# Optimization experiments

Measured on AMD Instinct MI355X. Metric: run time of the kernel, lower is better.

## Reference

```python
import jax, jax.numpy as jnp
import numpy as np
from jax.scipy.special import gammaln

TEMP = 1.0
PRIOR = 0.2
THRESHOLD = 0.5
EPS = 1e-12


def _normalize(x):
    # F.normalize: x / max(||x||_2, eps)
    n = jnp.linalg.norm(x, axis=-1, keepdims=True)
    return x / jnp.maximum(n, EPS)


def setup_inputs() -> dict:
    key = jax.random.key(0)
    k1, k2 = jax.random.split(key, 2)
    B, L, D = 8, 4096, 512
    hidden = jax.random.normal(k1, (B, L, D), dtype=jnp.float32)
    # uniform noise for RelaxedBernoulli rsample (probs shape is (B, L) after left-pad)
    noise = jax.random.uniform(k2, (B, L), dtype=jnp.float32, minval=1e-6, maxval=1.0 - 1e-6)
    # learned projections, initialized to identity as in the module
    q_w = jnp.eye(D, dtype=jnp.float32)
    k_w = jnp.eye(D, dtype=jnp.float32)
    return {"hidden": hidden, "q_w": q_w, "k_w": k_w, "noise": noise}


def reference(hidden, q_w, k_w, noise):
    B, L, D = hidden.shape
    # cosine-similarity boundary scoring between adjacent tokens
    q = _normalize(hidden[:, :-1]) @ q_w.T  # (B, L-1, D)
    k = _normalize(hidden[:, 1:]) @ k_w.T   # (B, L-1, D)
    cos_sim = jnp.einsum('bld,bld->bl', q, k)  # (B, L-1)
    probs = jnp.clip((1.0 - cos_sim) / 2.0, 0.0, 1.0)
    probs = jnp.pad(probs, ((0, 0), (1, 0)), constant_values=1.0)  # (B, L), first pos always boundary

    # RelaxedBernoulli rsample: sigmoid((logits + logistic_noise) / temp)
    logits = jnp.log(probs) - jnp.log1p(-probs)
    lnoise = jnp.log(noise) - jnp.log1p(-noise)
    soft_boundaries = jax.nn.sigmoid((logits + lnoise) / TEMP)

    # straight-through hard threshold
    hard_f = (soft_boundaries > THRESHOLD).astype(soft_boundaries.dtype)
    hard_boundaries = hard_f - jax.lax.stop_gradient(soft_boundaries) + soft_boundaries

    # dynamic segment pooling (`delete`): segment id = cumsum(boundaries) - 1,
    # mean-pool tokens of each segment; output padded to L segments.
    seg = jnp.clip(jnp.cumsum(hard_boundaries, axis=1).astype(jnp.int32) - 1, 0, L - 1)  # (B, L)

    def pool_one(h, s):
        sums = jax.ops.segment_sum(h, s, num_segments=L)                       # (L, D)
        cnts = jax.ops.segment_sum(jnp.ones((h.shape[0],), h.dtype), s, num_segments=L)
        return sums / jnp.maximum(cnts, 1.0)[:, None]

    pooled = jax.vmap(pool_one)(hidden, seg)   # (B, L, D) (empty segments are zeros)
    pooled = pooled.transpose(1, 0, 2)          # (L, B, D) per `.transpose(0, 1)`

    # Binomial(n=L, p=prior) log-prob loss on number of boundaries per row
    n = jnp.asarray(L, dtype=hidden.dtype)
    ksum = hard_boundaries.sum(axis=-1)  # (B,)
    log_prob = (gammaln(n + 1.0) - gammaln(ksum + 1.0) - gammaln(n - ksum + 1.0)
                + ksum * jnp.log(jnp.asarray(PRIOR, hidden.dtype))
                + (n - ksum) * jnp.log1p(-jnp.asarray(PRIOR, hidden.dtype)))
    loss = -jnp.mean(log_prob) / n
    return pooled, loss
```

## Files before the change

### kernel.cpp

```cpp
#include <hip/hip_runtime.h>
#include <hip/hip_bf16.h>
#include <math.h>

#define B_ 8
#define L_ 4096
#define D_ 512
#define STRIP 8
#define NWAVE (B_ * L_ / STRIP)

typedef float f4 __attribute__((ext_vector_type(4)));


__device__ __forceinline__ float wave_reduce_add(float v) {
#pragma unroll
    for (int o = 32; o > 0; o >>= 1) v += __shfl_xor(v, o, 64);
    return v;
}

__device__ __forceinline__ int wave_reduce_add_i(int v) {
#pragma unroll
    for (int o = 32; o > 0; o >>= 1) v += __shfl_xor(v, o, 64);
    return v;
}

__device__ __noinline__ unsigned long long general_strip(
    int b, int t0, const float* __restrict__ hidden, const float* __restrict__ noise,
    const float* __restrict__ q_w, const float* __restrict__ k_w, float* lds_wave,
    int lane) {
    const float* base = hidden + (size_t)b * L_ * D_;
    int i0 = lane * 4, i1 = lane * 4 + 256;
    int rp = (t0 > 0) ? (t0 - 1) : 0;

    f4 pa = *(const f4*)(base + (size_t)rp * D_ + i0);
    f4 pb = *(const f4*)(base + (size_t)rp * D_ + i1);
    float ssl;
    {
        float s = pa.x * pa.x + pa.y * pa.y + pa.z * pa.z + pa.w * pa.w;
        float s2 = pb.x * pb.x + pb.y * pb.y + pb.z * pb.z + pb.w * pb.w;
        ssl = wave_reduce_add(s + s2);
    }
    unsigned long long mask = 0;
    for (int i = 0; i < STRIP; ++i) {
        int l = t0 + i;
        unsigned char h;
        const float* rc = base + (size_t)l * D_;
        f4 ca = *(const f4*)(rc + i0);
        f4 cb = *(const f4*)(rc + i1);
        float ssr = (ca.x * ca.x + ca.y * ca.y + ca.z * ca.z + ca.w * ca.w) +
                    (cb.x * cb.x + cb.y * cb.y + cb.z * cb.z + cb.w * cb.w);
        ssr = wave_reduce_add(ssr);
        if (l == 0) {
            h = 1;
        } else {
            float nl = fmaxf(sqrtf(ssl), 1e-12f);
            float nr = fmaxf(sqrtf(ssr), 1e-12f);
            float* nL = lds_wave;
            float* nR = nL + D_;
            nL[i0 + 0] = pa.x / nl; nL[i0 + 1] = pa.y / nl;
            nL[i0 + 2] = pa.z / nl; nL[i0 + 3] = pa.w / nl;
            nL[i1 + 0] = pb.x / nl; nL[i1 + 1] = pb.y / nl;
            nL[i1 + 2] = pb.z / nl; nL[i1 + 3] = pb.w / nl;
            nR[i0 + 0] = ca.x / nr; nR[i0 + 1] = ca.y / nr;
            nR[i0 + 2] = ca.z / nr; nR[i0 + 3] = ca.w / nr;
            nR[i1 + 0] = cb.x / nr; nR[i1 + 1] = cb.y / nr;
            nR[i1 + 2] = cb.z / nr; nR[i1 + 3] = cb.w / nr;
            float acc = 0.f;
            for (int r8 = 0; r8 < 8; ++r8) {
                int row = lane + 64 * r8;
                float qi = 0.f, ki = 0.f;
                for (int j = 0; j < D_; ++j) {
                    qi += q_w[row * D_ + j] * nL[j];
                    ki += k_w[row * D_ + j] * nR[j];
                }
                acc += qi * ki;
            }
            float cosv = wave_reduce_add(acc);
            float p = fminf(fmaxf(0.5f * (1.0f - cosv), 0.0f), 1.0f);
            float u = noise[b * L_ + l];
            float x = (logf(p) - log1pf(-p)) + (logf(u) - log1pf(-u));
            float sg = 1.0f / (1.0f + expf(-x));
            h = (sg > 0.5f) ? (unsigned char)1 : (unsigned char)0;
        }
        mask |= ((unsigned long long)h) << (8 * i);
        pa = ca; pb = cb; ssl = ssr;
    }
    return mask;
}

__global__ __launch_bounds__(256, 4) void k_main(const float* __restrict__ hidden,
                                                 const float* __restrict__ noise,
                                                 const float* __restrict__ q_w,
                                                 const float* __restrict__ k_w,
                                                 int* __restrict__ nonid_arr,
                                                 unsigned long long* __restrict__ hard64) {
    int bid = blockIdx.x, tid = threadIdx.x;
    int wid = tid >> 6, lane = tid & 63;
    __shared__ unsigned long long sb[4];

    {
        int i = bid * 256 + tid;
        int rr = i >> 9, c = i & (D_ - 1);
        float e = (rr == c) ? 1.0f : 0.0f;
        bool bad = (q_w[i] != e) || (k_w[i] != e);
        unsigned long long m = __ballot(bad);
        if (lane == 0) sb[wid] = m;
        __syncthreads();
        if (tid == 0)
            nonid_arr[bid] = ((sb[0] | sb[1] | sb[2] | sb[3]) != 0ull) ? 1 : 0;
    }

    int wave = bid * 4 + wid;
    int b = wave >> 9;
    int t0 = (wave & 511) * STRIP;
    const float* base = hidden + (size_t)b * L_ * D_;
    int i0 = lane * 4, i1 = lane * 4 + 256;
    int rp = (t0 > 0) ? (t0 - 1) : 0;

    f4 A[9], Bv[9];
#pragma unroll
    for (int i = 0; i < 9; ++i) {
        int rr = (i == 0) ? rp : (t0 + i - 1);
        const float* rc = base + (size_t)rr * D_;
        A[i] = *(const f4*)(rc + i0);
        Bv[i] = *(const f4*)(rc + i1);
    }
    float ss0 = (A[0].x * A[0].x + A[0].y * A[0].y + A[0].z * A[0].z + A[0].w * A[0].w) +
                (Bv[0].x * Bv[0].x + Bv[0].y * Bv[0].y + Bv[0].z * Bv[0].z + Bv[0].w * Bv[0].w);
    float dp[STRIP], sp[STRIP];
#pragma unroll
    for (int i = 0; i < STRIP; ++i) {
        dp[i] = (A[i].x * A[i + 1].x + A[i].y * A[i + 1].y +
                 A[i].z * A[i + 1].z + A[i].w * A[i + 1].w) +
                (Bv[i].x * Bv[i + 1].x + Bv[i].y * Bv[i + 1].y +
                 Bv[i].z * Bv[i + 1].z + Bv[i].w * Bv[i + 1].w);
        sp[i] = (A[i + 1].x * A[i + 1].x + A[i + 1].y * A[i + 1].y +
                 A[i + 1].z * A[i + 1].z + A[i + 1].w * A[i + 1].w) +
                (Bv[i + 1].x * Bv[i + 1].x + Bv[i + 1].y * Bv[i + 1].y +
                 Bv[i + 1].z * Bv[i + 1].z + Bv[i + 1].w * Bv[i + 1].w);
    }
    float ss0r = wave_reduce_add(ss0);
#pragma unroll
    for (int i = 0; i < STRIP; ++i) {
        dp[i] = wave_reduce_add(dp[i]);
        sp[i] = wave_reduce_add(sp[i]);
    }
    float myDp = dp[7], mySsr = sp[7], mySsl = sp[6];
#pragma unroll
    for (int i = 0; i < 7; ++i) {
        if (lane == i) {
            myDp = dp[i];
            mySsr = sp[i];
            mySsl = (i == 0) ? ss0r : sp[i - 1];
        }
    }
    float u = noise[b * L_ + t0 + (lane & 7)];
    float nl = fmaxf(sqrtf(mySsl), 1e-12f);
    float nr = fmaxf(sqrtf(mySsr), 1e-12f);
    float cosv = myDp / (nl * nr);
    float p = fminf(fmaxf(0.5f * (1.0f - cosv), 0.0f), 1.0f);
    float x = (logf(p) - log1pf(-p)) + (logf(u) - log1pf(-u));
    float sg = 1.0f / (1.0f + expf(-x));
    unsigned long long bm = __ballot(sg > 0.5f);
    if (lane == 0) {
        unsigned long long m = 0;
#pragma unroll
        for (int i = 0; i < 8; ++i) m |= ((bm >> i) & 1ull) << (8 * i);
        if (t0 == 0) m = (m & ~0xFFull) | 1ull;
        hard64[wave] = m;
    }
}

__global__ __launch_bounds__(256) void k_scanpool(const float* __restrict__ hidden,
                                                  unsigned long long* hard64_arg,
                                                  const int* __restrict__ nonid_arr,
                                                  const float* __restrict__ noise,
                                                  const float* __restrict__ q_w,
                                                  const float* __restrict__ k_w,
                                                  float* __restrict__ out,
                                                  float* __restrict__ out_loss) {
    unsigned long long* hard64 = hard64_arg;
    const unsigned char* hard = (const unsigned char*)hard64_arg;
    int bx = blockIdx.x, b = blockIdx.y;
    int tid = threadIdx.x, wid = tid >> 6, lane = tid & 63;
    __shared__ int seg_lds[L_];
    __shared__ int wtot[4];
    __shared__ int sbw[4];
    __shared__ int s_S, s_nonid;

    {
        int4 nf = ((const int4*)nonid_arr)[tid];
        bool bad = __any((nf.x | nf.y | nf.z | nf.w) != 0);
        if (lane == 0) sbw[wid] = bad ? 1 : 0;
        __syncthreads();
        if (tid == 0) s_nonid = sbw[0] | sbw[1] | sbw[2] | sbw[3];
        __syncthreads();
    }
    if (s_nonid) {
        float* ldsw = (float*)seg_lds + wid * 2 * D_;
        for (int strip = wid; strip < L_ / STRIP; strip += 4) {
            unsigned long long m = general_strip(b, strip * STRIP, hidden, noise,
                                                 q_w, k_w, ldsw, lane);
            if (lane == 0) hard64[b * (L_ / STRIP) + strip] = m;
        }
        __syncthreads();
    }

    uint4 v = ((const uint4*)(hard + b * L_))[tid];
    int s = __popc(v.x) + __popc(v.y) + __popc(v.z) + __popc(v.w);
    int incl = s;
#pragma unroll
    for (int off = 1; off < 64; off <<= 1) {
        int t = __shfl_up(incl, off, 64);
        if (lane >= off) incl += t;
    }
    if (lane == 63) wtot[wid] = incl;
    __syncthreads();
    int woff = 0;
#pragma unroll
    for (int k = 0; k < 4; ++k)
        if (k < wid) woff += wtot[k];
    int run = woff + incl - s;
    int pbase = tid * 16;
    unsigned wds[4] = {v.x, v.y, v.z, v.w};
#pragma unroll
    for (int wi = 0; wi < 4; ++wi)
#pragma unroll
        for (int byte = 0; byte < 4; ++byte)
            if ((wds[wi] >> (8 * byte)) & 1) {
                run++;
                seg_lds[run - 1] = pbase + wi * 4 + byte;
            }
    if (tid == 255) s_S = woff + incl;
    __syncthreads();
    int S = s_S;

    int i0 = lane * 4, i1 = i0 + 256;
    for (int k = 0; k < 8; ++k) {
        int j = bx + 128 * (wid * 8 + k);
        f4 a0 = (f4)(0.0f);
        f4 a1 = (f4)(0.0f);
        if (j < S) {
            int start = seg_lds[j];
            int end = (j + 1 < S) ? seg_lds[j + 1] : L_;
            const float* base = hidden + ((size_t)b * L_ + start) * D_;
            for (int t = start; t < end; ++t, base += D_) {
                a0 += *(const f4*)(base + i0);
                a1 += *(const f4*)(base + i1);
            }
            float len = (float)(end - start);
            a0.x /= len; a0.y /= len; a0.z /= len; a0.w /= len;
            a1.x /= len; a1.y /= len; a1.z /= len; a1.w /= len;
        }
        float* o = out + ((size_t)j * B_ + b) * D_;
        __builtin_nontemporal_store(a0, (f4*)(o + i0));
        __builtin_nontemporal_store(a1, (f4*)(o + i1));
    }

    if (bx == 0 && b == 0) {
        __shared__ int ksum_lds[8];
        __shared__ int wsum[4];
        __shared__ double sh[17];
        for (int bb = 0; bb < 8; ++bb) {
            uint4 vv = ((const uint4*)(hard + bb * L_))[tid];
            int ss = __popc(vv.x) + __popc(vv.y) + __popc(vv.z) + __popc(vv.w);
            ss = wave_reduce_add_i(ss);
            if (lane == 0) wsum[wid] = ss;
            __syncthreads();
            if (tid == 0) ksum_lds[bb] = wsum[0] + wsum[1] + wsum[2] + wsum[3];
            __syncthreads();
        }
        double n = (double)L_;
        if (tid < 8) sh[tid] = lgamma((double)ksum_lds[tid] + 1.0);
        else if (tid < 16) sh[tid] = lgamma(n - (double)ksum_lds[tid - 8] + 1.0);
        else if (tid == 16) sh[16] = lgamma(n + 1.0);
        __syncthreads();
        if (tid == 0) {
            double acc = 0.0, lg = sh[16];
            for (int bb = 0; bb < 8; ++bb) {
                double k = (double)ksum_lds[bb];
                acc += lg - sh[bb] - sh[8 + bb] + k * log(0.2) + (n - k) * log(0.8);
            }
            out_loss[0] = (float)(-(acc / 8.0) / n);
        }
    }
}

extern "C" void kernel_launch(void* const* d_in, const int* in_sizes, int n_in,
                              void* d_out, int out_size, void* d_ws, size_t ws_size,
                              hipStream_t stream) {
    const float* hidden = (const float*)d_in[0];
    const float* q_w = (const float*)d_in[1];
    const float* k_w = (const float*)d_in[2];
    const float* noise = (const float*)d_in[3];
    float* out = (float*)d_out;
    float* out_loss = out + (size_t)L_ * B_ * D_;

    char* ws = (char*)d_ws;
    int* nonid_arr = (int*)(ws + 0);
    unsigned long long* hard64 = (unsigned long long*)(ws + 4096);

    k_main<<<NWAVE / 4, 256, 0, stream>>>(hidden, noise, q_w, k_w, nonid_arr, hard64);
    k_scanpool<<<dim3(L_ / 32, B_), 256, 0, stream>>>(hidden, hard64, nonid_arr, noise,
                                                      q_w, k_w, out, out_loss);
}
```

Before: 43.93 us.

## Split fused scan-pool kernel into per-batch scan and wide pooling kernels

The combined scan+pool kernel, where each of 1024 blocks redundantly recomputed the per-batch prefix scan, is split in two. A small kernel with 8 blocks scans each batch row once and writes segment starts and boundary counts to workspace. A second kernel with 8192 blocks pools one segment per wave and reads the counts directly, so the loss no longer recomputes popcounts. Nontemporal stores become plain stores. This removes the redundant scans and the serial per-wave loop in exchange for an extra launch and a global round trip for the segment starts.

```diff
diff --git a/kernel.cpp b/kernel.cpp
--- a/kernel.cpp
+++ b/kernel.cpp
@@ -12,12 +12,6 @@
 
 
 __device__ __forceinline__ float wave_reduce_add(float v) {
-#pragma unroll
-    for (int o = 32; o > 0; o >>= 1) v += __shfl_xor(v, o, 64);
-    return v;
-}
-
-__device__ __forceinline__ int wave_reduce_add_i(int v) {
 #pragma unroll
     for (int o = 32; o > 0; o >>= 1) v += __shfl_xor(v, o, 64);
     return v;
@@ -170,39 +164,37 @@
     }
 }
 
-__global__ __launch_bounds__(256) void k_scanpool(const float* __restrict__ hidden,
-                                                  unsigned long long* hard64_arg,
-                                                  const int* __restrict__ nonid_arr,
-                                                  const float* __restrict__ noise,
-                                                  const float* __restrict__ q_w,
-                                                  const float* __restrict__ k_w,
-                                                  float* __restrict__ out,
-                                                  float* __restrict__ out_loss) {
+__global__ __launch_bounds__(256) void k_scan(const float* __restrict__ hidden,
+                                              unsigned long long* hard64_arg,
+                                              const int* __restrict__ nonid_arr,
+                                              const float* __restrict__ noise,
+                                              const float* __restrict__ q_w,
+                                              const float* __restrict__ k_w,
+                                              int* __restrict__ seg_starts,
+                                              int* __restrict__ ksum) {
     unsigned long long* hard64 = hard64_arg;
     const unsigned char* hard = (const unsigned char*)hard64_arg;
-    int bx = blockIdx.x, b = blockIdx.y;
+    int b = blockIdx.x;
     int tid = threadIdx.x, wid = tid >> 6, lane = tid & 63;
-    __shared__ int seg_lds[L_];
+    __shared__ float ldsw_all[4 * 2 * D_];
     __shared__ int wtot[4];
     __shared__ int sbw[4];
-    __shared__ int s_S, s_nonid;
 
     {
         int4 nf = ((const int4*)nonid_arr)[tid];
         bool bad = __any((nf.x | nf.y | nf.z | nf.w) != 0);
         if (lane == 0) sbw[wid] = bad ? 1 : 0;
         __syncthreads();
-        if (tid == 0) s_nonid = sbw[0] | sbw[1] | sbw[2] | sbw[3];
-        __syncthreads();
-    }
-    if (s_nonid) {
-        float* ldsw = (float*)seg_lds + wid * 2 * D_;
-        for (int strip = wid; strip < L_ / STRIP; strip += 4) {
-            unsigned long long m = general_strip(b, strip * STRIP, hidden, noise,
-                                                 q_w, k_w, ldsw, lane);
-            if (lane == 0) hard64[b * (L_ / STRIP) + strip] = m;
-        }
-        __syncthreads();
+        int nonid = sbw[0] | sbw[1] | sbw[2] | sbw[3];
+        if (nonid) {
+            float* ldsw = ldsw_all + wid * 2 * D_;
+            for (int strip = wid; strip < L_ / STRIP; strip += 4) {
+                unsigned long long m = general_strip(b, strip * STRIP, hidden, noise,
+                                                     q_w, k_w, ldsw, lane);
+                if (lane == 0) hard64[b * (L_ / STRIP) + strip] = m;
+            }
+            __syncthreads();
+        }
     }
 
     uint4 v = ((const uint4*)(hard + b * L_))[tid];
@@ -228,56 +220,50 @@
         for (int byte = 0; byte < 4; ++byte)
             if ((wds[wi] >> (8 * byte)) & 1) {
                 run++;
-                seg_lds[run - 1] = pbase + wi * 4 + byte;
-            }
-    if (tid == 255) s_S = woff + incl;
-    __syncthreads();
-    int S = s_S;
-
+                seg_starts[b * L_ + run - 1] = pbase + wi * 4 + byte;
+            }
+    if (tid == 255) ksum[b] = woff + incl;
+}
+
+__global__ __launch_bounds__(256) void k_pool(const float* __restrict__ hidden,
+                                              const int* __restrict__ seg_starts,
+                                              const int* __restrict__ ksum,
+                                              float* __restrict__ out,
+                                              float* __restrict__ out_loss) {
+    int bx = blockIdx.x, b = blockIdx.y;
+    int tid = threadIdx.x, wid = tid >> 6, lane = tid & 63;
+    int j = bx + 1024 * wid;
+    int S = ksum[b];
     int i0 = lane * 4, i1 = i0 + 256;
-    for (int k = 0; k < 8; ++k) {
-        int j = bx + 128 * (wid * 8 + k);
-        f4 a0 = (f4)(0.0f);
-        f4 a1 = (f4)(0.0f);
-        if (j < S) {
-            int start = seg_lds[j];
-            int end = (j + 1 < S) ? seg_lds[j + 1] : L_;
-            const float* base = hidden + ((size_t)b * L_ + start) * D_;
-            for (int t = start; t < end; ++t, base += D_) {
-                a0 += *(const f4*)(base + i0);
-                a1 += *(const f4*)(base + i1);
-            }
-            float len = (float)(end - start);
-            a0.x /= len; a0.y /= len; a0.z /= len; a0.w /= len;
-            a1.x /= len; a1.y /= len; a1.z /= len; a1.w /= len;
-        }
-        float* o = out + ((size_t)j * B_ + b) * D_;
-        __builtin_nontemporal_store(a0, (f4*)(o + i0));
-        __builtin_nontemporal_store(a1, (f4*)(o + i1));
-    }
+    f4 a0 = (f4)(0.0f);
+    f4 a1 = (f4)(0.0f);
+    if (j < S) {
+        int start = seg_starts[b * L_ + j];
+        int end = (j + 1 < S) ? seg_starts[b * L_ + j + 1] : L_;
+        const float* base = hidden + ((size_t)b * L_ + start) * D_;
+        for (int t = start; t < end; ++t, base += D_) {
+            a0 += *(const f4*)(base + i0);
+            a1 += *(const f4*)(base + i1);
+        }
+        float len = (float)(end - start);
+        a0.x /= len; a0.y /= len; a0.z /= len; a0.w /= len;
+        a1.x /= len; a1.y /= len; a1.z /= len; a1.w /= len;
+    }
+    float* o = out + ((size_t)j * B_ + b) * D_;
+    *(f4*)(o + i0) = a0;
+    *(f4*)(o + i1) = a1;
 
     if (bx == 0 && b == 0) {
-        __shared__ int ksum_lds[8];
-        __shared__ int wsum[4];
         __shared__ double sh[17];
-        for (int bb = 0; bb < 8; ++bb) {
-            uint4 vv = ((const uint4*)(hard + bb * L_))[tid];
-            int ss = __popc(vv.x) + __popc(vv.y) + __popc(vv.z) + __popc(vv.w);
-            ss = wave_reduce_add_i(ss);
-            if (lane == 0) wsum[wid] = ss;
-            __syncthreads();
-            if (tid == 0) ksum_lds[bb] = wsum[0] + wsum[1] + wsum[2] + wsum[3];
-            __syncthreads();
-        }
         double n = (double)L_;
-        if (tid < 8) sh[tid] = lgamma((double)ksum_lds[tid] + 1.0);
-        else if (tid < 16) sh[tid] = lgamma(n - (double)ksum_lds[tid - 8] + 1.0);
+        if (tid < 8) sh[tid] = lgamma((double)ksum[tid] + 1.0);
+        else if (tid < 16) sh[tid] = lgamma(n - (double)ksum[tid - 8] + 1.0);
         else if (tid == 16) sh[16] = lgamma(n + 1.0);
         __syncthreads();
         if (tid == 0) {
             double acc = 0.0, lg = sh[16];
             for (int bb = 0; bb < 8; ++bb) {
-                double k = (double)ksum_lds[bb];
+                double k = (double)ksum[bb];
                 acc += lg - sh[bb] - sh[8 + bb] + k * log(0.2) + (n - k) * log(0.8);
             }
             out_loss[0] = (float)(-(acc / 8.0) / n);
@@ -298,8 +284,11 @@
     char* ws = (char*)d_ws;
     int* nonid_arr = (int*)(ws + 0);
     unsigned long long* hard64 = (unsigned long long*)(ws + 4096);
+    int* seg_starts = (int*)(ws + 36864);
+    int* ksum = (int*)(ws + 167936);
 
     k_main<<<NWAVE / 4, 256, 0, stream>>>(hidden, noise, q_w, k_w, nonid_arr, hard64);
-    k_scanpool<<<dim3(L_ / 32, B_), 256, 0, stream>>>(hidden, hard64, nonid_arr, noise,
-                                                      q_w, k_w, out, out_loss);
-}
+    k_scan<<<B_, 256, 0, stream>>>(hidden, hard64, nonid_arr, noise, q_w, k_w,
+                                   seg_starts, ksum);
+    k_pool<<<dim3(1024, B_), 256, 0, stream>>>(hidden, seg_starts, ksum, out, out_loss);
+}
```

After: 43.71 us. About the same (-0.5%).
